# Optimization experiments

Measured on AMD Instinct MI355X. Metric: run time of the kernel, lower is better.

The kernel has to match this reference:

```python
import jax, jax.numpy as jnp
import numpy as np

NEG_SLOPE = 0.01

def setup_inputs() -> dict:
    key = jax.random.key(0)
    ks = jax.random.split(key, 6)
    B, N, IN, OUT = 4, 4096, 256, 128
    x = jax.random.normal(ks[0], (B, N, IN), dtype=jnp.float32)
    # fc: Linear(in, out, bias=False); attn_l/attn_r: Linear(out, 1) with bias
    W_fc = jax.random.normal(ks[1], (IN, OUT), dtype=jnp.float32) / np.sqrt(IN)
    w_l = jax.random.normal(ks[2], (OUT,), dtype=jnp.float32) / np.sqrt(OUT)
    b_l = jax.random.normal(ks[3], (), dtype=jnp.float32) * 0.01
    w_r = jax.random.normal(ks[4], (OUT,), dtype=jnp.float32) / np.sqrt(OUT)
    b_r = jax.random.normal(ks[5], (), dtype=jnp.float32) * 0.01
    return {"x": x, "W_fc": W_fc, "w_l": w_l, "b_l": b_l, "w_r": w_r, "b_r": b_r}

def reference(x, W_fc, w_l, b_l, w_r, b_r):
    # feats: [B, N, OUT]
    feats = jnp.einsum('bni,io->bno', x, W_fc)
    f1 = jnp.einsum('bno,o->bn', feats, w_l) + b_l  # [B, N]
    f2 = jnp.einsum('bno,o->bn', feats, w_r) + b_r  # [B, N]
    # logits[b, i, j] = f1[b, i] + f2[b, j]  (broadcast-add)
    logits = f1[:, :, None] + f2[:, None, :]        # [B, N, N]
    scores = jnp.where(logits >= 0, logits, NEG_SLOPE * logits)
    coefs = jax.nn.softmax(scores, axis=1)          # softmax over dim=1, as in torch code
    return jnp.einsum('bij,bjo->bio', coefs, feats) # [B, N, OUT]
```

## Files before the change

### kernel.cpp

```cpp
#include <hip/hip_runtime.h>

using u16 = unsigned short;
using u32 = unsigned int;
using u64 = unsigned long long;

typedef short bf16x8 __attribute__((ext_vector_type(8)));
typedef float f32x4 __attribute__((ext_vector_type(4)));

static constexpr int NB  = 4;
static constexpr int NN  = 4096;
static constexpr int KIN = 256;
static constexpr int FO  = 128;
static constexpr int NROW = NB * NN;
static constexpr int NCC = 64;
static constexpr float SLOPE = 0.01f;

__device__ __forceinline__ u16 f2bf(float f) {
  const u32 u = __float_as_uint(f);
  return (u16)((u + 0x7fffu + ((u >> 16) & 1u)) >> 16);
}
__device__ __forceinline__ float bf2f(u16 h) {
  return __uint_as_float(((u32)h) << 16);
}
__device__ __forceinline__ float dot4(const float4& a, const float4& b) {
  return a.x * b.x + a.y * b.y + a.z * b.z + a.w * b.w;
}

__device__ __forceinline__ u32 f2key(float f) {
  const u32 b = __float_as_uint(f);
  return (b & 0x80000000u) ? ~b : (b | 0x80000000u);
}
__device__ __forceinline__ float key2f(u32 u) {
  const u32 b = (u & 0x80000000u) ? (u ^ 0x80000000u) : ~u;
  return __uint_as_float(b);
}

__device__ __forceinline__ u64 shfl_xor64(u64 v, int m) {
  const u32 lo = __shfl_xor((u32)(v & 0xffffffffu), m, 64);
  const u32 hi = __shfl_xor((u32)(v >> 32), m, 64);
  return ((u64)hi << 32) | (u64)lo;
}
__device__ __forceinline__ void cswap(u64& a, u64& b, bool up) {
  if ((a > b) == up) { const u64 tmp = a; a = b; b = tmp; }
}

__device__ __forceinline__ void reg_session(u64 e[4], int t, int k) {
  const int jstart = (k > 256) ? 128 : (k >> 1);
  for (int j = jstart; j >= 4; j >>= 1) {
    const int J = j >> 2;
    const bool up   = ((t & (k >> 2)) == 0);
    const bool lowr = ((t & J) == 0);
#pragma unroll
    for (int r = 0; r < 4; ++r) {
      const u64 o = shfl_xor64(e[r], J);
      const bool less = e[r] < o;
      e[r] = ((lowr == up) == less) ? e[r] : o;
    }
  }
  if (k >= 4) {
    const bool up = ((t & (k >> 2)) == 0);
    cswap(e[0], e[2], up); cswap(e[1], e[3], up);
  }
  {
    const bool up0 = (((4 * t)     & k) == 0);
    const bool up1 = (((4 * t + 2) & k) == 0);
    cswap(e[0], e[1], up0); cswap(e[2], e[3], up1);
  }
}

__device__ __forceinline__ int lower_bound_g(const float* __restrict__ a, int n, float t) {
  int lo = 0, hi = n;
  while (lo < hi) {
    const int mid = (lo + hi) >> 1;
    if (a[mid] < t) lo = mid + 1; else hi = mid;
  }
  return lo;
}

__global__ __launch_bounds__(256) void k0_prep(const float* __restrict__ W,
                                               const float* __restrict__ wl,
                                               const float* __restrict__ wr,
                                               float* __restrict__ u_l,
                                               float* __restrict__ u_r,
                                               u16* __restrict__ whT,
                                               u16* __restrict__ wloT,
                                               int* __restrict__ cnt) {
  const int t = threadIdx.x;
  const int blk = blockIdx.x;
  if (blk == 0 && t < NB) cnt[t] = 0;
  if (blk < 64) {
    const int k = blk * 4 + (t >> 6);
    const int lane = t & 63;
    const float w0 = W[k * FO + lane], w1 = W[k * FO + 64 + lane];
    float a1 = w0 * wl[lane] + w1 * wl[64 + lane];
    float a2 = w0 * wr[lane] + w1 * wr[64 + lane];
#pragma unroll
    for (int off = 1; off < 64; off <<= 1) {
      a1 += __shfl_xor(a1, off, 64);
      a2 += __shfl_xor(a2, off, 64);
    }
    if (lane == 0) { u_l[k] = a1; u_r[k] = a2; }
  } else {
#pragma unroll
    for (int e = 0; e < 2; ++e) {
      const int idx = (blk - 64) * 512 + t + e * 256;
      const int col = idx >> 8, k = idx & 255;
      const float v = W[k * FO + col];
      const u16 h = f2bf(v);
      whT[col * KIN + k]  = h;
      wloT[col * KIN + k] = f2bf(v - bf2f(h));
    }
  }
}

__global__ __launch_bounds__(256) void k1_fused(const float* __restrict__ x,
                                                const u16* __restrict__ whT,
                                                const u16* __restrict__ wloT,
                                                const float* __restrict__ u_l,
                                                const float* __restrict__ u_r,
                                                const float* __restrict__ blp,
                                                const float* __restrict__ brp,
                                                float* __restrict__ feats,
                                                float* __restrict__ f1g,
                                                float* __restrict__ f2g) {
  __shared__ u16 axh[64][72];
  __shared__ u16 axl[64][72];
  __shared__ u16 bwh[128][72];
  __shared__ u16 bwl[128][72];
  const int t = threadIdx.x;
  const int w = t >> 6, lane = t & 63;
  const int wm = w >> 1, wn = w & 1;
  const int row0 = blockIdx.x * 64;
  const int xr = t >> 3, xc = t & 7;
  f32x4 acc[2][4];
#pragma unroll
  for (int m = 0; m < 2; ++m)
#pragma unroll
    for (int n = 0; n < 4; ++n) acc[m][n] = (f32x4)0.f;

  float d1a = 0.f, d2a = 0.f, d1b = 0.f, d2b = 0.f;
  float4 xa0, xa1, xb0, xb1;
  bf16x8 wh_[4], wl_[4];

  {
    const float* pa = x + (size_t)(row0 + xr) * KIN + xc * 8;
    const float* pb = x + (size_t)(row0 + xr + 32) * KIN + xc * 8;
    xa0 = *(const float4*)pa; xa1 = *(const float4*)(pa + 4);
    xb0 = *(const float4*)pb; xb1 = *(const float4*)(pb + 4);
#pragma unroll
    for (int i = 0; i < 4; ++i) {
      const int v = t + i * 256;
      const int col = v >> 3, c = v & 7;
      wh_[i] = *(const bf16x8*)(whT + (size_t)col * KIN + c * 8);
      wl_[i] = *(const bf16x8*)(wloT + (size_t)col * KIN + c * 8);
    }
  }

  for (int it = 0; it < 4; ++it) {
    if (it) __syncthreads();
    {
      const float4 ul0 = *(const float4*)(u_l + it * 64 + xc * 8);
      const float4 ul1 = *(const float4*)(u_l + it * 64 + xc * 8 + 4);
      const float4 ur0 = *(const float4*)(u_r + it * 64 + xc * 8);
      const float4 ur1 = *(const float4*)(u_r + it * 64 + xc * 8 + 4);
      d1a += dot4(xa0, ul0) + dot4(xa1, ul1);
      d2a += dot4(xa0, ur0) + dot4(xa1, ur1);
      d1b += dot4(xb0, ul0) + dot4(xb1, ul1);
      d2b += dot4(xb0, ur0) + dot4(xb1, ur1);
    }
    {
      float va[8] = {xa0.x, xa0.y, xa0.z, xa0.w, xa1.x, xa1.y, xa1.z, xa1.w};
      float vb[8] = {xb0.x, xb0.y, xb0.z, xb0.w, xb1.x, xb1.y, xb1.z, xb1.w};
      bf16x8 ha, la, hb, lb;
#pragma unroll
      for (int q = 0; q < 8; ++q) {
        const u16 h1 = f2bf(va[q]);
        ha[q] = (short)h1; la[q] = (short)f2bf(va[q] - bf2f(h1));
        const u16 h2 = f2bf(vb[q]);
        hb[q] = (short)h2; lb[q] = (short)f2bf(vb[q] - bf2f(h2));
      }
      *(bf16x8*)(&axh[xr][xc * 8]) = ha;
      *(bf16x8*)(&axl[xr][xc * 8]) = la;
      *(bf16x8*)(&axh[xr + 32][xc * 8]) = hb;
      *(bf16x8*)(&axl[xr + 32][xc * 8]) = lb;
    }
#pragma unroll
    for (int i = 0; i < 4; ++i) {
      const int v = t + i * 256;
      const int col = v >> 3, c = v & 7;
      *(bf16x8*)(&bwh[col][c * 8]) = wh_[i];
      *(bf16x8*)(&bwl[col][c * 8]) = wl_[i];
    }
    __syncthreads();
    if (it < 3) {
      const float* pa = x + (size_t)(row0 + xr) * KIN + (it + 1) * 64 + xc * 8;
      const float* pb = x + (size_t)(row0 + xr + 32) * KIN + (it + 1) * 64 + xc * 8;
      xa0 = *(const float4*)pa; xa1 = *(const float4*)(pa + 4);
      xb0 = *(const float4*)pb; xb1 = *(const float4*)(pb + 4);
#pragma unroll
      for (int i = 0; i < 4; ++i) {
        const int v = t + i * 256;
        const int col = v >> 3, c = v & 7;
        wh_[i] = *(const bf16x8*)(whT + (size_t)col * KIN + (it + 1) * 64 + c * 8);
        wl_[i] = *(const bf16x8*)(wloT + (size_t)col * KIN + (it + 1) * 64 + c * 8);
      }
    }
#pragma unroll
    for (int kk = 0; kk < 2; ++kk) {
      const int kb = kk * 32 + (lane >> 4) * 8;
      bf16x8 ah[2], al[2], bh[4], blo[4];
#pragma unroll
      for (int m = 0; m < 2; ++m) {
        const int r = wm * 32 + m * 16 + (lane & 15);
        ah[m] = *(const bf16x8*)(&axh[r][kb]);
        al[m] = *(const bf16x8*)(&axl[r][kb]);
      }
#pragma unroll
      for (int n = 0; n < 4; ++n) {
        const int cidx = wn * 64 + n * 16 + (lane & 15);
        bh[n]  = *(const bf16x8*)(&bwh[cidx][kb]);
        blo[n] = *(const bf16x8*)(&bwl[cidx][kb]);
      }
#pragma unroll
      for (int m = 0; m < 2; ++m)
#pragma unroll
        for (int n = 0; n < 4; ++n) {
          acc[m][n] = __builtin_amdgcn_mfma_f32_16x16x32_bf16(ah[m], bh[n],  acc[m][n], 0, 0, 0);
          acc[m][n] = __builtin_amdgcn_mfma_f32_16x16x32_bf16(ah[m], blo[n], acc[m][n], 0, 0, 0);
          acc[m][n] = __builtin_amdgcn_mfma_f32_16x16x32_bf16(al[m], bh[n],  acc[m][n], 0, 0, 0);
        }
    }
  }

#pragma unroll
  for (int m = 0; m < 2; ++m) {
    const int rb = row0 + wm * 32 + m * 16 + (lane >> 4) * 4;
    const int cb = wn * 64 + (lane & 15);
#pragma unroll
    for (int n = 0; n < 4; ++n)
#pragma unroll
      for (int r = 0; r < 4; ++r)
        feats[(size_t)(rb + r) * FO + cb + n * 16] = acc[m][n][r];
  }

#pragma unroll
  for (int off = 1; off < 8; off <<= 1) {
    d1a += __shfl_xor(d1a, off, 64);
    d2a += __shfl_xor(d2a, off, 64);
    d1b += __shfl_xor(d1b, off, 64);
    d2b += __shfl_xor(d2b, off, 64);
  }
  if ((t & 7) == 0) {
    const float bl = blp[0], br = brp[0];
    f1g[row0 + xr] = d1a + bl;
    f2g[row0 + xr] = d2a + br;
    f1g[row0 + xr + 32] = d1b + bl;
    f2g[row0 + xr + 32] = d2b + br;
  }
}

__global__ __launch_bounds__(1024, 1) void k3a_sort(const float* __restrict__ f1g,
                                                    const float* __restrict__ f2g,
                                                    float* __restrict__ f1sort,
                                                    float* __restrict__ sc1,
                                                    float* __restrict__ sc2,
                                                    float* __restrict__ f2sort,
                                                    int* __restrict__ jidxS) {
  __shared__ u64 lds[NN];
  __shared__ float wsumA[16], wsumB[16];
  const int t = threadIdx.x;
  const int lane = t & 63, wv = t >> 6;
  const int b = blockIdx.x & 3;
  const int task = blockIdx.x >> 2;
  const int base = b * NN;
  const float* __restrict__ src = task ? f2g : f1g;

  u64 e[4];
#pragma unroll
  for (int r = 0; r < 4; ++r) {
    const int i = 4 * t + r;
    e[r] = ((u64)f2key(src[base + i]) << 32) | (u32)i;
  }

  for (int k = 2; k <= 256; k <<= 1) reg_session(e, t, k);
#pragma unroll
  for (int r = 0; r < 4; ++r) lds[4 * t + r] = e[r];
  __syncthreads();

  for (int k = 512; k <= NN; k <<= 1) {
    for (int j = k >> 1; j >= 256; j >>= 1) {
#pragma unroll
      for (int pp = 0; pp < 2; ++pp) {
        const int p = t + pp * 1024;
        const int i = ((p & ~(j - 1)) << 1) | (p & (j - 1));
        const int ix = i | j;
        const bool up = ((i & k) == 0);
        const u64 a = lds[i], c = lds[ix];
        if ((a > c) == up) { lds[i] = c; lds[ix] = a; }
      }
      __syncthreads();
    }
#pragma unroll
    for (int r = 0; r < 4; ++r) e[r] = lds[4 * t + r];
    reg_session(e, t, k);
    if (k < NN) {
#pragma unroll
      for (int r = 0; r < 4; ++r) lds[4 * t + r] = e[r];
      __syncthreads();
    }
  }

  if (task == 0) {
    float kf[4], a[4], c[4];
#pragma unroll
    for (int r = 0; r < 4; ++r) {
      kf[r] = key2f((u32)(e[r] >> 32));
      f1sort[base + 4 * t + r] = kf[r];
      a[r] = expf(kf[r]);
      c[r] = expf(SLOPE * kf[r]);
    }
#pragma unroll
    for (int r = 1; r < 4; ++r) { a[r] += a[r - 1]; c[r] += c[r - 1]; }
    const float sa = a[3], sb = c[3];
    float pa = sa, pb = sb;
    for (int off = 1; off < 64; off <<= 1) {
      const float oa = __shfl_up(pa, off, 64);
      const float ob = __shfl_up(pb, off, 64);
      if (lane >= off) { pa += oa; pb += ob; }
    }
    if (lane == 63) { wsumA[wv] = pa; wsumB[wv] = pb; }
    __syncthreads();
    float wpa = 0.f, wpb = 0.f;
    for (int w2 = 0; w2 < wv; ++w2) { wpa += wsumA[w2]; wpb += wsumB[w2]; }
    const float basea = wpa + pa - sa, baseb = wpb + pb - sb;
#pragma unroll
    for (int r = 0; r < 4; ++r) {
      sc1[base + 4 * t + r] = basea + a[r];
      sc2[base + 4 * t + r] = baseb + c[r];
    }
  } else {
#pragma unroll
    for (int r = 0; r < 4; ++r) {
      f2sort[base + 4 * t + r] = key2f((u32)(e[r] >> 32));
      jidxS[base + 4 * t + r]  = (int)(e[r] & 0xffffffffu);
    }
  }
}

__global__ __launch_bounds__(128) void k4a_pref(const float* __restrict__ feats,
                                                const float* __restrict__ f1sort,
                                                const float* __restrict__ sc1,
                                                const float* __restrict__ sc2,
                                                const float* __restrict__ f2sort,
                                                const float* __restrict__ f1g,
                                                const int* __restrict__ jidxS,
                                                float* __restrict__ finePreA,
                                                float* __restrict__ finePreB,
                                                int* __restrict__ kposA,
                                                float* __restrict__ E1g,
                                                float* __restrict__ E2g,
                                                float* __restrict__ coarA,
                                                float* __restrict__ coarB,
                                                int* __restrict__ cnt) {
  __shared__ float sal[64], sbe[64];
  __shared__ int s_last;
  const int b = blockIdx.x >> 6, cc = blockIdx.x & 63;
  const int tid = threadIdx.x;
  const int bb = b * NN;
  const int base = bb + cc * 64;

  if (tid < 64) {
    const int pos = cc * 64 + tid;
    const float T1 = sc1[bb + NN - 1];
    const float f1max = f1sort[bb + NN - 1];
    const float f2v = f2sort[bb + pos];
    const float m = f1max + f2v;
    const float M = (m >= 0.f) ? m : SLOPE * m;
    const int pp = lower_bound_g(f1sort + bb, NN, -f2v);
    const float S1 = T1 - (pp > 0 ? sc1[bb + pp - 1] : 0.f);
    const float S2 = (pp > 0 ? sc2[bb + pp - 1] : 0.f);
    const float ea = expf(f2v - M);
    const float eb = expf(SLOPE * f2v - M);
    const float invD = 1.0f / (ea * S1 + eb * S2);
    sal[tid] = ea * invD;
    sbe[tid] = eb * invD;
  } else {
    const int row = cc * 64 + (tid - 64);
    const float f1v = f1g[bb + row];
    kposA[bb + row] = lower_bound_g(f2sort + bb, NN, -f1v);
    E1g[bb + row] = expf(f1v);
    E2g[bb + row] = expf(SLOPE * f1v);
  }
  __syncthreads();

  {
    const int o = tid;
    const float* fb = feats + (size_t)b * NN * FO;
    float accA = 0.f, accB = 0.f;
#pragma unroll 8
    for (int q = 0; q < 64; ++q) {
      const int kk = base + q;
      const int j = jidxS[kk];
      const float fv = fb[(size_t)j * FO + o];
      accA = fmaf(sal[q], fv, accA);
      accB = fmaf(sbe[q], fv, accB);
      finePreA[(size_t)kk * FO + o] = accA;
      finePreB[(size_t)kk * FO + o] = accB;
    }
  }

  __syncthreads();
  if (tid == 0) {
    __threadfence();
    s_last = (atomicAdd(&cnt[b], 1) == NCC - 1) ? 1 : 0;
  }
  __syncthreads();
  if (s_last) {
    __threadfence();
    const int o = tid;
    float runA = 0.f, runB = 0.f;
#pragma unroll 8
    for (int c = 0; c < NCC; ++c) {
      coarA[(size_t)(b * (NCC + 1) + c) * FO + o] = runA;
      coarB[(size_t)(b * (NCC + 1) + c) * FO + o] = runB;
      runA += finePreA[(size_t)(b * NN + c * 64 + 63) * FO + o];
      runB += finePreB[(size_t)(b * NN + c * 64 + 63) * FO + o];
    }
    coarA[(size_t)(b * (NCC + 1) + NCC) * FO + o] = runA;
    coarB[(size_t)(b * (NCC + 1) + NCC) * FO + o] = runB;
  }
}

__global__ __launch_bounds__(256) void k5_out(const float* __restrict__ finePreA,
                                              const float* __restrict__ finePreB,
                                              const float* __restrict__ coarA,
                                              const float* __restrict__ coarB,
                                              const int* __restrict__ kposA,
                                              const float* __restrict__ E1g,
                                              const float* __restrict__ E2g,
                                              float* __restrict__ out) {
  const int t = threadIdx.x;
  const int row = blockIdx.x * 2 + (t >> 7);
  const int o = t & 127;
  const int b = row >> 12;
  const int kp = kposA[row];
  const float e1 = E1g[row], e2 = E2g[row];
  const int c = kp >> 6;

  float runA = coarA[(size_t)(b * (NCC + 1) + c) * FO + o];
  float runB = coarB[(size_t)(b * (NCC + 1) + c) * FO + o];
  const float totA = coarA[(size_t)(b * (NCC + 1) + NCC) * FO + o];
  if (kp & 63) {
    runA += finePreA[(size_t)(b * NN + kp - 1) * FO + o];
    runB += finePreB[(size_t)(b * NN + kp - 1) * FO + o];
  }
  out[(size_t)row * FO + o] = fmaf(e1, totA - runA, e2 * runB);
}

extern "C" void kernel_launch(void* const* d_in, const int* in_sizes, int n_in,
                              void* d_out, int out_size, void* d_ws, size_t ws_size,
                              hipStream_t stream) {
  const float* x  = (const float*)d_in[0];
  const float* W  = (const float*)d_in[1];
  const float* wl = (const float*)d_in[2];
  const float* bl = (const float*)d_in[3];
  const float* wr = (const float*)d_in[4];
  const float* br = (const float*)d_in[5];
  float* out = (float*)d_out;

  float* ws = (float*)d_ws;
  float* feats    = ws; ws += NROW * FO;
  float* finePreA = ws; ws += NROW * FO;
  float* finePreB = ws; ws += NROW * FO;
  float* f1g      = ws; ws += NROW;
  float* f2g      = ws; ws += NROW;
  float* f1sort   = ws; ws += NROW;
  float* f2sort   = ws; ws += NROW;
  float* sc1      = ws; ws += NROW;
  float* sc2      = ws; ws += NROW;
  float* E1g      = ws; ws += NROW;
  float* E2g      = ws; ws += NROW;
  int* jidxS      = (int*)ws; ws += NROW;
  int* kposA      = (int*)ws; ws += NROW;
  float* coarA    = ws; ws += NB * (NCC + 1) * FO;
  float* coarB    = ws; ws += NB * (NCC + 1) * FO;
  float* u_l      = ws; ws += KIN;
  float* u_r      = ws; ws += KIN;
  u16* whT  = (u16*)ws; ws += FO * KIN / 2;
  u16* wloT = (u16*)ws; ws += FO * KIN / 2;
  int* cnt  = (int*)ws; ws += NB;
  (void)in_sizes; (void)n_in; (void)out_size; (void)ws_size;

  hipLaunchKernelGGL(k0_prep,  dim3(128),       dim3(256),  0, stream,
                     W, wl, wr, u_l, u_r, whT, wloT, cnt);
  hipLaunchKernelGGL(k1_fused, dim3(NROW / 64), dim3(256),  0, stream,
                     x, whT, wloT, u_l, u_r, bl, br, feats, f1g, f2g);
  hipLaunchKernelGGL(k3a_sort, dim3(8),         dim3(1024), 0, stream,
                     f1g, f2g, f1sort, sc1, sc2, f2sort, jidxS);
  hipLaunchKernelGGL(k4a_pref, dim3(NB * NCC),  dim3(128),  0, stream,
                     feats, f1sort, sc1, sc2, f2sort, f1g, jidxS,
                     finePreA, finePreB, kposA, E1g, E2g, coarA, coarB, cnt);
  hipLaunchKernelGGL(k5_out,   dim3(NROW / 2),  dim3(256),  0, stream,
                     finePreA, finePreB, coarA, coarB, kposA, E1g, E2g, out);
}
```

Before: 75.82 us.

## Fold weight prep into GEMM kernel, halve prefix chunk size, split coarse scan kernel

Removes the k0_prep kernel. Every k1 block now computes the W·w_l and W·w_r projections and converts W into hi/lo bf16 halves in shared memory itself, which saves a launch but repeats that work in all 256 blocks. The prefix kernel moves to 32-row chunks (128 chunks per batch) for more parallelism and shorter serial loops. The atomic last-block coarse scan is replaced by a separate small k4c kernel, which drops the counter and threadfence at the cost of an extra launch and a longer serial coarse scan.

Result: no change. 74.54 us (-1.7%).

```diff
diff --git a/kernel.cpp b/kernel.cpp
--- a/kernel.cpp
+++ b/kernel.cpp
@@ -12,7 +12,8 @@
 static constexpr int KIN = 256;
 static constexpr int FO  = 128;
 static constexpr int NROW = NB * NN;
-static constexpr int NCC = 64;
+static constexpr int NCC = 128;
+static constexpr int CH  = 32;
 static constexpr float SLOPE = 0.01f;
 
 __device__ __forceinline__ u16 f2bf(float f) {
@@ -77,56 +78,21 @@
   return lo;
 }
 
-__global__ __launch_bounds__(256) void k0_prep(const float* __restrict__ W,
-                                               const float* __restrict__ wl,
-                                               const float* __restrict__ wr,
-                                               float* __restrict__ u_l,
-                                               float* __restrict__ u_r,
-                                               u16* __restrict__ whT,
-                                               u16* __restrict__ wloT,
-                                               int* __restrict__ cnt) {
-  const int t = threadIdx.x;
-  const int blk = blockIdx.x;
-  if (blk == 0 && t < NB) cnt[t] = 0;
-  if (blk < 64) {
-    const int k = blk * 4 + (t >> 6);
-    const int lane = t & 63;
-    const float w0 = W[k * FO + lane], w1 = W[k * FO + 64 + lane];
-    float a1 = w0 * wl[lane] + w1 * wl[64 + lane];
-    float a2 = w0 * wr[lane] + w1 * wr[64 + lane];
-#pragma unroll
-    for (int off = 1; off < 64; off <<= 1) {
-      a1 += __shfl_xor(a1, off, 64);
-      a2 += __shfl_xor(a2, off, 64);
-    }
-    if (lane == 0) { u_l[k] = a1; u_r[k] = a2; }
-  } else {
-#pragma unroll
-    for (int e = 0; e < 2; ++e) {
-      const int idx = (blk - 64) * 512 + t + e * 256;
-      const int col = idx >> 8, k = idx & 255;
-      const float v = W[k * FO + col];
-      const u16 h = f2bf(v);
-      whT[col * KIN + k]  = h;
-      wloT[col * KIN + k] = f2bf(v - bf2f(h));
-    }
-  }
-}
-
-__global__ __launch_bounds__(256) void k1_fused(const float* __restrict__ x,
-                                                const u16* __restrict__ whT,
-                                                const u16* __restrict__ wloT,
-                                                const float* __restrict__ u_l,
-                                                const float* __restrict__ u_r,
-                                                const float* __restrict__ blp,
-                                                const float* __restrict__ brp,
-                                                float* __restrict__ feats,
-                                                float* __restrict__ f1g,
-                                                float* __restrict__ f2g) {
+__global__ __launch_bounds__(256) void k1_all(const float* __restrict__ x,
+                                              const float* __restrict__ W,
+                                              const float* __restrict__ wlp,
+                                              const float* __restrict__ blp,
+                                              const float* __restrict__ wrp,
+                                              const float* __restrict__ brp,
+                                              float* __restrict__ feats,
+                                              float* __restrict__ f1g,
+                                              float* __restrict__ f2g) {
   __shared__ u16 axh[64][72];
   __shared__ u16 axl[64][72];
   __shared__ u16 bwh[128][72];
   __shared__ u16 bwl[128][72];
+  __shared__ float uls[KIN];
+  __shared__ float urs[KIN];
   const int t = threadIdx.x;
   const int w = t >> 6, lane = t & 63;
   const int wm = w >> 1, wn = w & 1;
@@ -140,33 +106,37 @@
 
   float d1a = 0.f, d2a = 0.f, d1b = 0.f, d2b = 0.f;
   float4 xa0, xa1, xb0, xb1;
-  bf16x8 wh_[4], wl_[4];
 
   {
     const float* pa = x + (size_t)(row0 + xr) * KIN + xc * 8;
     const float* pb = x + (size_t)(row0 + xr + 32) * KIN + xc * 8;
     xa0 = *(const float4*)pa; xa1 = *(const float4*)(pa + 4);
     xb0 = *(const float4*)pb; xb1 = *(const float4*)(pb + 4);
-#pragma unroll
-    for (int i = 0; i < 4; ++i) {
-      const int v = t + i * 256;
-      const int col = v >> 3, c = v & 7;
-      wh_[i] = *(const bf16x8*)(whT + (size_t)col * KIN + c * 8);
-      wl_[i] = *(const bf16x8*)(wloT + (size_t)col * KIN + c * 8);
-    }
-  }
+  }
+  {
+    const float* Wr = W + (size_t)t * FO;
+    float s1 = 0.f, s2 = 0.f;
+#pragma unroll 8
+    for (int c = 0; c < FO; ++c) {
+      const float wv = Wr[c];
+      s1 = fmaf(wv, wlp[c], s1);
+      s2 = fmaf(wv, wrp[c], s2);
+    }
+    uls[t] = s1; urs[t] = s2;
+  }
+
+  const int wcol = t & 127;
+  const int wrh = t >> 7;
 
   for (int it = 0; it < 4; ++it) {
     if (it) __syncthreads();
-    {
-      const float4 ul0 = *(const float4*)(u_l + it * 64 + xc * 8);
-      const float4 ul1 = *(const float4*)(u_l + it * 64 + xc * 8 + 4);
-      const float4 ur0 = *(const float4*)(u_r + it * 64 + xc * 8);
-      const float4 ur1 = *(const float4*)(u_r + it * 64 + xc * 8 + 4);
-      d1a += dot4(xa0, ul0) + dot4(xa1, ul1);
-      d2a += dot4(xa0, ur0) + dot4(xa1, ur1);
-      d1b += dot4(xb0, ul0) + dot4(xb1, ul1);
-      d2b += dot4(xb0, ur0) + dot4(xb1, ur1);
+#pragma unroll 8
+    for (int pss = 0; pss < 32; ++pss) {
+      const int k = pss * 2 + wrh;
+      const float v = W[(size_t)(it * 64 + k) * FO + wcol];
+      const u16 h = f2bf(v);
+      bwh[wcol][k] = h;
+      bwl[wcol][k] = f2bf(v - bf2f(h));
     }
     {
       float va[8] = {xa0.x, xa0.y, xa0.z, xa0.w, xa1.x, xa1.y, xa1.z, xa1.w};
@@ -184,26 +154,22 @@
       *(bf16x8*)(&axh[xr + 32][xc * 8]) = hb;
       *(bf16x8*)(&axl[xr + 32][xc * 8]) = lb;
     }
-#pragma unroll
-    for (int i = 0; i < 4; ++i) {
-      const int v = t + i * 256;
-      const int col = v >> 3, c = v & 7;
-      *(bf16x8*)(&bwh[col][c * 8]) = wh_[i];
-      *(bf16x8*)(&bwl[col][c * 8]) = wl_[i];
-    }
     __syncthreads();
+    {
+      const float4 ul0 = *(const float4*)(&uls[it * 64 + xc * 8]);
+      const float4 ul1 = *(const float4*)(&uls[it * 64 + xc * 8 + 4]);
+      const float4 ur0 = *(const float4*)(&urs[it * 64 + xc * 8]);
+      const float4 ur1 = *(const float4*)(&urs[it * 64 + xc * 8 + 4]);
+      d1a += dot4(xa0, ul0) + dot4(xa1, ul1);
+      d2a += dot4(xa0, ur0) + dot4(xa1, ur1);
+      d1b += dot4(xb0, ul0) + dot4(xb1, ul1);
+      d2b += dot4(xb0, ur0) + dot4(xb1, ur1);
+    }
     if (it < 3) {
       const float* pa = x + (size_t)(row0 + xr) * KIN + (it + 1) * 64 + xc * 8;
       const float* pb = x + (size_t)(row0 + xr + 32) * KIN + (it + 1) * 64 + xc * 8;
       xa0 = *(const float4*)pa; xa1 = *(const float4*)(pa + 4);
       xb0 = *(const float4*)pb; xb1 = *(const float4*)(pb + 4);
-#pragma unroll
-      for (int i = 0; i < 4; ++i) {
-        const int v = t + i * 256;
-        const int col = v >> 3, c = v & 7;
-        wh_[i] = *(const bf16x8*)(whT + (size_t)col * KIN + (it + 1) * 64 + c * 8);
-        wl_[i] = *(const bf16x8*)(wloT + (size_t)col * KIN + (it + 1) * 64 + c * 8);
-      }
     }
 #pragma unroll
     for (int kk = 0; kk < 2; ++kk) {
@@ -358,19 +324,15 @@
                                                 float* __restrict__ finePreB,
                                                 int* __restrict__ kposA,
                                                 float* __restrict__ E1g,
-                                                float* __restrict__ E2g,
-                                                float* __restrict__ coarA,
-                                                float* __restrict__ coarB,
-                                                int* __restrict__ cnt) {
-  __shared__ float sal[64], sbe[64];
-  __shared__ int s_last;
-  const int b = blockIdx.x >> 6, cc = blockIdx.x & 63;
+                                                float* __restrict__ E2g) {
+  __shared__ float sal[CH], sbe[CH];
+  const int b = blockIdx.x >> 7, cc = blockIdx.x & 127;
   const int tid = threadIdx.x;
   const int bb = b * NN;
-  const int base = bb + cc * 64;
-
-  if (tid < 64) {
-    const int pos = cc * 64 + tid;
+  const int base = bb + cc * CH;
+
+  if (tid < CH) {
+    const int pos = cc * CH + tid;
     const float T1 = sc1[bb + NN - 1];
     const float f1max = f1sort[bb + NN - 1];
     const float f2v = f2sort[bb + pos];
@@ -384,8 +346,8 @@
     const float invD = 1.0f / (ea * S1 + eb * S2);
     sal[tid] = ea * invD;
     sbe[tid] = eb * invD;
-  } else {
-    const int row = cc * 64 + (tid - 64);
+  } else if (tid < 2 * CH) {
+    const int row = cc * CH + (tid - CH);
     const float f1v = f1g[bb + row];
     kposA[bb + row] = lower_bound_g(f2sort + bb, NN, -f1v);
     E1g[bb + row] = expf(f1v);
@@ -393,42 +355,37 @@
   }
   __syncthreads();
 
-  {
-    const int o = tid;
-    const float* fb = feats + (size_t)b * NN * FO;
-    float accA = 0.f, accB = 0.f;
+  const int o = tid;
+  const float* fb = feats + (size_t)b * NN * FO;
+  float accA = 0.f, accB = 0.f;
 #pragma unroll 8
-    for (int q = 0; q < 64; ++q) {
-      const int kk = base + q;
-      const int j = jidxS[kk];
-      const float fv = fb[(size_t)j * FO + o];
-      accA = fmaf(sal[q], fv, accA);
-      accB = fmaf(sbe[q], fv, accB);
-      finePreA[(size_t)kk * FO + o] = accA;
-      finePreB[(size_t)kk * FO + o] = accB;
-    }
-  }
-
-  __syncthreads();
-  if (tid == 0) {
-    __threadfence();
-    s_last = (atomicAdd(&cnt[b], 1) == NCC - 1) ? 1 : 0;
-  }
-  __syncthreads();
-  if (s_last) {
-    __threadfence();
-    const int o = tid;
-    float runA = 0.f, runB = 0.f;
+  for (int q = 0; q < CH; ++q) {
+    const int kk = base + q;
+    const int j = jidxS[kk];
+    const float fv = fb[(size_t)j * FO + o];
+    accA = fmaf(sal[q], fv, accA);
+    accB = fmaf(sbe[q], fv, accB);
+    finePreA[(size_t)kk * FO + o] = accA;
+    finePreB[(size_t)kk * FO + o] = accB;
+  }
+}
+
+__global__ __launch_bounds__(128) void k4c_coar(const float* __restrict__ finePreA,
+                                                const float* __restrict__ finePreB,
+                                                float* __restrict__ coarA,
+                                                float* __restrict__ coarB) {
+  const int b = blockIdx.x;
+  const int o = threadIdx.x;
+  float runA = 0.f, runB = 0.f;
 #pragma unroll 8
-    for (int c = 0; c < NCC; ++c) {
-      coarA[(size_t)(b * (NCC + 1) + c) * FO + o] = runA;
-      coarB[(size_t)(b * (NCC + 1) + c) * FO + o] = runB;
-      runA += finePreA[(size_t)(b * NN + c * 64 + 63) * FO + o];
-      runB += finePreB[(size_t)(b * NN + c * 64 + 63) * FO + o];
-    }
-    coarA[(size_t)(b * (NCC + 1) + NCC) * FO + o] = runA;
-    coarB[(size_t)(b * (NCC + 1) + NCC) * FO + o] = runB;
-  }
+  for (int c = 0; c < NCC; ++c) {
+    coarA[(size_t)(b * (NCC + 1) + c) * FO + o] = runA;
+    coarB[(size_t)(b * (NCC + 1) + c) * FO + o] = runB;
+    runA += finePreA[(size_t)(b * NN + c * CH + CH - 1) * FO + o];
+    runB += finePreB[(size_t)(b * NN + c * CH + CH - 1) * FO + o];
+  }
+  coarA[(size_t)(b * (NCC + 1) + NCC) * FO + o] = runA;
+  coarB[(size_t)(b * (NCC + 1) + NCC) * FO + o] = runB;
 }
 
 __global__ __launch_bounds__(256) void k5_out(const float* __restrict__ finePreA,
@@ -445,12 +402,12 @@
   const int b = row >> 12;
   const int kp = kposA[row];
   const float e1 = E1g[row], e2 = E2g[row];
-  const int c = kp >> 6;
+  const int c = kp >> 5;
 
   float runA = coarA[(size_t)(b * (NCC + 1) + c) * FO + o];
   float runB = coarB[(size_t)(b * (NCC + 1) + c) * FO + o];
   const float totA = coarA[(size_t)(b * (NCC + 1) + NCC) * FO + o];
-  if (kp & 63) {
+  if (kp & 31) {
     runA += finePreA[(size_t)(b * NN + kp - 1) * FO + o];
     runB += finePreB[(size_t)(b * NN + kp - 1) * FO + o];
   }
@@ -484,22 +441,17 @@
   int* kposA      = (int*)ws; ws += NROW;
   float* coarA    = ws; ws += NB * (NCC + 1) * FO;
   float* coarB    = ws; ws += NB * (NCC + 1) * FO;
-  float* u_l      = ws; ws += KIN;
-  float* u_r      = ws; ws += KIN;
-  u16* whT  = (u16*)ws; ws += FO * KIN / 2;
-  u16* wloT = (u16*)ws; ws += FO * KIN / 2;
-  int* cnt  = (int*)ws; ws += NB;
   (void)in_sizes; (void)n_in; (void)out_size; (void)ws_size;
 
-  hipLaunchKernelGGL(k0_prep,  dim3(128),       dim3(256),  0, stream,
-                     W, wl, wr, u_l, u_r, whT, wloT, cnt);
-  hipLaunchKernelGGL(k1_fused, dim3(NROW / 64), dim3(256),  0, stream,
-                     x, whT, wloT, u_l, u_r, bl, br, feats, f1g, f2g);
+  hipLaunchKernelGGL(k1_all,   dim3(NROW / 64), dim3(256),  0, stream,
+                     x, W, wl, bl, wr, br, feats, f1g, f2g);
   hipLaunchKernelGGL(k3a_sort, dim3(8),         dim3(1024), 0, stream,
                      f1g, f2g, f1sort, sc1, sc2, f2sort, jidxS);
   hipLaunchKernelGGL(k4a_pref, dim3(NB * NCC),  dim3(128),  0, stream,
                      feats, f1sort, sc1, sc2, f2sort, f1g, jidxS,
-                     finePreA, finePreB, kposA, E1g, E2g, coarA, coarB, cnt);
+                     finePreA, finePreB, kposA, E1g, E2g);
+  hipLaunchKernelGGL(k4c_coar, dim3(NB),        dim3(128),  0, stream,
+                     finePreA, finePreB, coarA, coarB);
   hipLaunchKernelGGL(k5_out,   dim3(NROW / 2),  dim3(256),  0, stream,
                      finePreA, finePreB, coarA, coarB, kposA, E1g, E2g, out);
 }
```
